# Kernel optimization log

Hardware: AMD Instinct MI355X
Metric: run time of the kernel (lower is better)

The kernel has to match this reference:

```python
import math
import jax, jax.numpy as jnp
import numpy as np
from jax import lax


def rotate_nearest(x, angle_deg):
    # x: (..., H, W); nearest-neighbor rotation about image center with expand=True
    H, W = x.shape[-2:]
    th = math.radians(angle_deg)
    c, s = math.cos(th), math.sin(th)
    nW = int(math.ceil(abs(W * c) + abs(H * s)))
    nH = int(math.ceil(abs(W * s) + abs(H * c)))
    cy, cx = (H - 1) * 0.5, (W - 1) * 0.5
    ncy, ncx = (nH - 1) * 0.5, (nW - 1) * 0.5
    yy, xx = jnp.meshgrid(jnp.arange(nH, dtype=jnp.float32), jnp.arange(nW, dtype=jnp.float32), indexing='ij')
    sx = c * (xx - ncx) - s * (yy - ncy) + cx
    sy = s * (xx - ncx) + c * (yy - ncy) + cy
    ix = jnp.clip(jnp.round(sx).astype(jnp.int32), 0, W - 1)
    iy = jnp.clip(jnp.round(sy).astype(jnp.int32), 0, H - 1)
    valid = (sx >= -0.5) & (sx <= W - 0.5) & (sy >= -0.5) & (sy <= H - 0.5)
    out = x[..., iy, ix]
    return jnp.where(valid, out, jnp.zeros((), dtype=x.dtype))


def scharr_gradients(img):
    # img: (B, C, H, W) -> (B, C, 2, H, W); cross-correlation like F.conv2d
    B, C, H, W = img.shape
    kx = jnp.array([[-3., 0., 3.], [10., 0., 10.], [-3., 0., 3.]], dtype=img.dtype)
    k = jnp.stack([kx, kx.T])[:, None]  # (2,1,3,3)
    y = lax.conv_general_dilated(img.reshape(B * C, 1, H, W), k, (1, 1), [(1, 1), (1, 1)],
                                 dimension_numbers=('NCHW', 'OIHW', 'NCHW'))
    return y.reshape(B, C, 2, H, W)


def rotated_xywh(img_height, img_width, angle=45.0):
    th = math.radians(angle)
    a, b = math.cos(th), math.sin(th)
    cx, cy = img_width / 2.0, img_height / 2.0
    rot = np.array([[a, b, (1 - a) * cx - b * cy], [-b, a, b * cx + (1 - a) * cy]])
    pts = np.array([[0, 0, 1], [img_width - 1, 0, 1], [0, img_height - 1, 1],
                    [img_width - 1, img_height - 1, 1]], dtype=np.float64)
    p = pts @ rot.T
    return (p[:, 0].min(), p[:, 1].min(), p[:, 0].max() - p[:, 0].min(), p[:, 1].max() - p[:, 1].min())


def gaussian_derivatives(img):
    # img: (C, H, W) -> (C, 8, H, W) : [grad+, grad-, rot_grad+, rot_grad-]
    C, H, W = img.shape
    g = scharr_gradients(img[None])[0]  # (C,2,H,W)
    xywh = rotated_xywh(H, W, 45.0)
    startx = int(max(0, (xywh[2] - W) / 2))
    starty = int(max(0, (xywh[3] - H) / 2))
    img_rot = rotate_nearest(img, 45.0)
    g_rot = scharr_gradients(img_rot[None])[0]
    g_rot = rotate_nearest(g_rot, -45.0)
    g_rot = g_rot[..., starty:starty + H, startx:startx + W]
    return jnp.concatenate([jnp.maximum(g, 0.0), jnp.minimum(g, 0.0),
                            jnp.maximum(g_rot, 0.0), jnp.minimum(g_rot, 0.0)], axis=-3)


def normalize_min_max(x):
    hmin = x.min(axis=(-2, -1), keepdims=True)
    hmax = x.max(axis=(-2, -1), keepdims=True)
    return (x - hmin) / (hmax - hmin)


def setup_inputs() -> dict:
    key = jax.random.key(0)
    k1, k2 = jax.random.split(key)
    img = jax.random.uniform(k1, (3, 1024, 1024), dtype=jnp.float32)
    reg_lab = jax.random.randint(k2, (1024, 1024), 0, 5000, dtype=jnp.int64)
    return {"img": img, "reg_lab": reg_lab, "nb_segs": 5000,
            "color_histogram_bins": 25, "texture_histogram_bins": 10}


def reference(img, reg_lab, nb_segs, color_histogram_bins, texture_histogram_bins):
    C, H, W = img.shape
    reg = reg_lab.reshape(-1).astype(jnp.int32)

    # per-region bounding boxes (vectorized segment min/max of pixel coords)
    yy, xx = jnp.meshgrid(jnp.arange(H, dtype=jnp.int32), jnp.arange(W, dtype=jnp.int32), indexing='ij')
    x_min = jax.ops.segment_min(xx.reshape(-1), reg, num_segments=nb_segs)
    y_min = jax.ops.segment_min(yy.reshape(-1), reg, num_segments=nb_segs)
    x_max = jax.ops.segment_max(xx.reshape(-1), reg, num_segments=nb_segs)
    y_max = jax.ops.segment_max(yy.reshape(-1), reg, num_segments=nb_segs)
    xywh = jnp.stack([x_min, y_min, x_max - x_min, y_max - y_min], axis=-1)  # (nb_segs, 4)

    region_sizes = jax.ops.segment_sum(jnp.ones_like(reg, jnp.float32), reg, num_segments=nb_segs)

    # color histograms
    cb = color_histogram_bins
    qc = (img * (cb - 1)).astype(jnp.int32)  # trunc == floor for x >= 0
    Zc = (reg_lab[None].astype(jnp.int32) * cb + qc).reshape(C, -1)
    hist_c = jax.vmap(lambda z: jax.ops.segment_sum(jnp.ones_like(z, jnp.float32), z, num_segments=nb_segs * cb))(Zc)
    color_hist = hist_c.reshape(C, nb_segs, cb).transpose(1, 0, 2)  # (nb_segs, C, cb)
    color_hist = color_hist / color_hist.sum(axis=(-2, -1), keepdims=True)

    # texture histograms over 8 gaussian-derivative channels
    tb = texture_histogram_bins
    deriv = normalize_min_max(gaussian_derivatives(img))  # (C, 8, H, W) in [0, 1]
    qt = (deriv * (tb - 1)).astype(jnp.int32)
    Zt = (reg_lab[None, None].astype(jnp.int32) * tb + qt).reshape(C * 8, -1)
    hist_t = jax.vmap(lambda z: jax.ops.segment_sum(jnp.ones_like(z, jnp.float32), z, num_segments=nb_segs * tb))(Zt)
    tex_hist = hist_t.reshape(C, 8, nb_segs, tb).transpose(2, 0, 1, 3)  # (nb_segs, C, 8, tb)
    tex_hist = tex_hist / tex_hist.sum(axis=(-3, -2, -1), keepdims=True)

    return xywh, region_sizes, color_hist, tex_hist
```

## Files before the change

### kernel.cpp

```cpp
#include <hip/hip_runtime.h>
#include <math.h>
#include <float.h>
#include <limits.h>

#define HH 1024
#define WW 1024
#define NPIX (HH*WW)
#define RH 1449
#define RW 1449
#define NBSEG 5000
#define START 211
#define NBLK_MM 2048

#define OUT_XYWH_OFF  0
#define OUT_SIZE_OFF  20000
#define OUT_COLOR_OFF 25000
#define OUT_TEX_OFF   400000
#define OUT_TOTAL     1600000


__global__ __launch_bounds__(256) void k_zero(int* __restrict__ cnt) {
  int i = blockIdx.x * 256 + threadIdx.x;
  if (i < 5120) cnt[i] = 0;
}

__global__ __launch_bounds__(256, 8) void k_mm(const float* __restrict__ img,
                                               const int* __restrict__ reg,
                                               int* __restrict__ cnt,
                                               int* __restrict__ rank,
                                               float4* __restrict__ grad4,
                                               float* __restrict__ pmin,
                                               float* __restrict__ pmax,
                                               float cb, float sb, float cf, float sf) {
  int tbase = blockIdx.x * 256 + threadIdx.x;
  float vmn[12], vmx[12];
  #pragma unroll
  for (int m = 0; m < 12; ++m) { vmn[m] = FLT_MAX; vmx[m] = -FLT_MAX; }

  #pragma unroll
  for (int k = 0; k < 2; ++k) {
    int p = tbase + k * (NPIX / 2);
    int y = p >> 10, x = p & (WW - 1);
    int s = reg[p];
    if ((unsigned)s < (unsigned)NBSEG) rank[p] = atomicAdd(&cnt[s], 1);

    float sx, sy;
    {
      #pragma clang fp contract(off)
      float dx = (float)(x + START) - 1024.5f;
      float dy = (float)(y + START) - 1024.5f;
      sx = cb*dx - sb*dy + 724.0f;
      sy = sb*dx + cb*dy + 724.0f;
    }
    bool valid2 = (sx >= -0.5f) && (sx <= (float)RW - 0.5f) &&
                  (sy >= -0.5f) && (sy <= (float)RH - 0.5f);
    int ix = min(max((int)rintf(sx), 0), RW - 1);
    int iy = min(max((int)rintf(sy), 0), RH - 1);

    float fxc, fyc;
    {
      #pragma clang fp contract(off)
      float ddx = (float)ix - 724.0f;
      float ddy = (float)iy - 724.0f;
      fxc = cf*ddx - sf*ddy + 511.5f;
      fyc = sf*ddx + cf*ddy + 511.5f;
    }

    int idxs[9];
    unsigned okm = 0;
    #pragma unroll
    for (int t = 0; t < 9; ++t) {
      const int dxi = (t % 3) - 1, dyi = (t / 3) - 1;
      int rx = ix + dxi, ry = iy + dyi;
      bool inside = ((unsigned)rx < (unsigned)RW) && ((unsigned)ry < (unsigned)RH);
      float fx = fxc + (cf*(float)dxi - sf*(float)dyi);
      float fy = fyc + (sf*(float)dxi + cf*(float)dyi);
      bool v1 = (fx >= -0.5f) && (fx <= 1023.5f) && (fy >= -0.5f) && (fy <= 1023.5f);
      int jx = min(max((int)rintf(fx), 0), WW - 1);
      int jy = min(max((int)rintf(fy), 0), HH - 1);
      idxs[t] = jy * WW + jx;
      okm |= ((unsigned)(inside && v1)) << t;
    }

    bool interior = (x >= 1) && (x <= WW - 2) && (y >= 1) && (y <= HH - 2);

    #pragma unroll
    for (int c = 0; c < 3; ++c) {
      const float* pp = img + (long)c * NPIX;
      float n00, n01, n02, n10, n12, n20, n21, n22;
      if (interior) {
        const float* q = pp + p;
        n00 = q[-WW - 1]; n01 = q[-WW]; n02 = q[-WW + 1];
        n10 = q[-1];                    n12 = q[1];
        n20 = q[WW - 1];  n21 = q[WW];  n22 = q[WW + 1];
      } else {
        bool yu = y > 0, yd = y < HH - 1, xl = x > 0, xr = x < WW - 1;
        n00 = (yu && xl) ? pp[p - WW - 1] : 0.0f;
        n01 = (yu)       ? pp[p - WW]     : 0.0f;
        n02 = (yu && xr) ? pp[p - WW + 1] : 0.0f;
        n10 = (xl)       ? pp[p - 1]      : 0.0f;
        n12 = (xr)       ? pp[p + 1]      : 0.0f;
        n20 = (yd && xl) ? pp[p + WW - 1] : 0.0f;
        n21 = (yd)       ? pp[p + WW]     : 0.0f;
        n22 = (yd && xr) ? pp[p + WW + 1] : 0.0f;
      }
      float a0 = -3.0f*n00 + 3.0f*n02 + 10.0f*n10 + 10.0f*n12 - 3.0f*n20 + 3.0f*n22;
      float a1 = -3.0f*n00 + 10.0f*n01 - 3.0f*n02 + 3.0f*n20 + 10.0f*n21 + 3.0f*n22;

      float m0, m1, m2, m3, m5, m6, m7, m8;
      m0 = (okm & 1u)   ? pp[idxs[0]] : 0.0f;
      m1 = (okm & 2u)   ? pp[idxs[1]] : 0.0f;
      m2 = (okm & 4u)   ? pp[idxs[2]] : 0.0f;
      m3 = (okm & 8u)   ? pp[idxs[3]] : 0.0f;
      m5 = (okm & 32u)  ? pp[idxs[5]] : 0.0f;
      m6 = (okm & 64u)  ? pp[idxs[6]] : 0.0f;
      m7 = (okm & 128u) ? pp[idxs[7]] : 0.0f;
      m8 = (okm & 256u) ? pp[idxs[8]] : 0.0f;
      float r0 = -3.0f*m0 + 3.0f*m2 + 10.0f*m3 + 10.0f*m5 - 3.0f*m6 + 3.0f*m8;
      float r1 = -3.0f*m0 + 10.0f*m1 - 3.0f*m2 + 3.0f*m6 + 10.0f*m7 + 3.0f*m8;
      float b0 = valid2 ? r0 : 0.0f;
      float b1 = valid2 ? r1 : 0.0f;

      grad4[(long)c * NPIX + p] = make_float4(a0, a1, b0, b1);

      vmn[2*c]     = fminf(vmn[2*c],     a0); vmx[2*c]     = fmaxf(vmx[2*c],     a0);
      vmn[2*c + 1] = fminf(vmn[2*c + 1], a1); vmx[2*c + 1] = fmaxf(vmx[2*c + 1], a1);
      vmn[6 + 2*c]     = fminf(vmn[6 + 2*c],     b0); vmx[6 + 2*c]     = fmaxf(vmx[6 + 2*c],     b0);
      vmn[6 + 2*c + 1] = fminf(vmn[6 + 2*c + 1], b1); vmx[6 + 2*c + 1] = fmaxf(vmx[6 + 2*c + 1], b1);
    }
  }

  #pragma unroll
  for (int off = 32; off >= 1; off >>= 1) {
    #pragma unroll
    for (int m = 0; m < 12; ++m) {
      vmn[m] = fminf(vmn[m], __shfl_xor(vmn[m], off));
      vmx[m] = fmaxf(vmx[m], __shfl_xor(vmx[m], off));
    }
  }
  __shared__ float smn[12][4], smx[12][4];
  int wv = threadIdx.x >> 6;
  if ((threadIdx.x & 63) == 0) {
    #pragma unroll
    for (int m = 0; m < 12; ++m) { smn[m][wv] = vmn[m]; smx[m][wv] = vmx[m]; }
  }
  __syncthreads();
  if (threadIdx.x < 12) {
    int m = threadIdx.x;
    float mn = fminf(fminf(smn[m][0], smn[m][1]), fminf(smn[m][2], smn[m][3]));
    float mx = fmaxf(fmaxf(smx[m][0], smx[m][1]), fmaxf(smx[m][2], smx[m][3]));
    pmin[m * NBLK_MM + blockIdx.x] = mn;
    pmax[m * NBLK_MM + blockIdx.x] = mx;
  }
}

__global__ __launch_bounds__(1024) void k_redscan(const float* __restrict__ pmin,
                                                  const float* __restrict__ pmax,
                                                  const int* __restrict__ cnt,
                                                  float* __restrict__ gmm,
                                                  int* __restrict__ start) {
  int t = threadIdx.x;
  if (blockIdx.x < 12) {
    int m = blockIdx.x;
    float mn = fminf(pmin[m * NBLK_MM + t], pmin[m * NBLK_MM + 1024 + t]);
    float mx = fmaxf(pmax[m * NBLK_MM + t], pmax[m * NBLK_MM + 1024 + t]);
    #pragma unroll
    for (int off = 32; off >= 1; off >>= 1) {
      mn = fminf(mn, __shfl_xor(mn, off));
      mx = fmaxf(mx, __shfl_xor(mx, off));
    }
    __shared__ float smn[16], smx[16];
    int wv = t >> 6;
    if ((t & 63) == 0) { smn[wv] = mn; smx[wv] = mx; }
    __syncthreads();
    if (t == 0) {
      #pragma unroll
      for (int i = 1; i < 16; ++i) { mn = fminf(mn, smn[i]); mx = fmaxf(mx, smx[i]); }
      gmm[2*m] = mn; gmm[2*m + 1] = mx;
    }
    return;
  }
  __shared__ int part[1024];
  int base = t * 5;
  int v[5]; int sum = 0;
  #pragma unroll
  for (int j = 0; j < 5; ++j) {
    v[j] = (base + j < NBSEG) ? cnt[base + j] : 0;
    sum += v[j];
  }
  part[t] = sum;
  __syncthreads();
  #pragma unroll
  for (int d = 1; d < 1024; d <<= 1) {
    int xv = (t >= d) ? part[t - d] : 0;
    __syncthreads();
    part[t] += xv;
    __syncthreads();
  }
  int run = (t > 0) ? part[t - 1] : 0;
  #pragma unroll
  for (int j = 0; j < 5; ++j) {
    int i = base + j;
    if (i <= NBSEG) start[i] = run;
    run += v[j];
  }
}

__global__ __launch_bounds__(256) void k_bin(const float* __restrict__ img,
                                             const int* __restrict__ reg,
                                             const int* __restrict__ rank,
                                             const int* __restrict__ start,
                                             const float* __restrict__ gmm,
                                             const float4* __restrict__ grad4,
                                             uint4* __restrict__ rec) {
  __shared__ float params[48];
  if (threadIdx.x < 24) {
    int t = threadIdx.x;
    int c = t / 8, k = t % 8;
    int b = (k < 4) ? (2*c + (k & 1)) : (6 + 2*c + (k & 1));
    bool pos = ((k >> 1) & 1) == 0;
    float mn = gmm[2*b], mx = gmm[2*b + 1];
    float hmin, hmax;
    if (pos) { hmin = fmaxf(mn, 0.0f); hmax = fmaxf(mx, 0.0f); }
    else     { hmin = fminf(mn, 0.0f); hmax = fminf(mx, 0.0f); }
    params[2*t]     = hmin;
    params[2*t + 1] = 9.0f / (hmax - hmin);
  }
  __syncthreads();

  int p = blockIdx.x * 256 + threadIdx.x;
  int s = reg[p];
  if ((unsigned)s >= (unsigned)NBSEG) return;

  unsigned q[24];
  #pragma unroll
  for (int c = 0; c < 3; ++c) {
    float4 g = grad4[(long)c * NPIX + p];
    float gv[2] = { g.x, g.y };
    float rv[2] = { g.z, g.w };
    #pragma unroll
    for (int d = 0; d < 2; ++d) {
      {
        int m = c*8 + d;
        float v = fmaxf(gv[d], 0.0f);
        int qq = (int)((v - params[2*m]) * params[2*m + 1]);
        q[m] = (unsigned)min(max(qq, 0), 9);
      }
      {
        int m = c*8 + 2 + d;
        float v = fminf(gv[d], 0.0f);
        int qq = (int)((v - params[2*m]) * params[2*m + 1]);
        q[m] = (unsigned)min(max(qq, 0), 9);
      }
      {
        int m = c*8 + 4 + d;
        float v = fmaxf(rv[d], 0.0f);
        int qq = (int)((v - params[2*m]) * params[2*m + 1]);
        q[m] = (unsigned)min(max(qq, 0), 9);
      }
      {
        int m = c*8 + 6 + d;
        float v = fminf(rv[d], 0.0f);
        int qq = (int)((v - params[2*m]) * params[2*m + 1]);
        q[m] = (unsigned)min(max(qq, 0), 9);
      }
    }
  }
  unsigned qc[3];
  #pragma unroll
  for (int c = 0; c < 3; ++c) {
    int cc = (int)(img[(long)c * NPIX + p] * 24.0f);
    qc[c] = (unsigned)min(max(cc, 0), 24);
  }

  unsigned trip[8];
  #pragma unroll
  for (int j = 0; j < 8; ++j)
    trip[j] = q[3*j] + 10u*q[3*j + 1] + 100u*q[3*j + 2];
  unsigned cp = qc[0] + 25u*qc[1] + 625u*qc[2];

  uint4 r;
  r.x = (unsigned)p | (trip[0] << 20);
  r.y = trip[1] | (trip[2] << 10) | (trip[3] << 20);
  r.z = trip[4] | (trip[5] << 10) | (trip[6] << 20);
  r.w = trip[7] | (cp << 10);

  rec[start[s] + rank[p]] = r;
}

__global__ __launch_bounds__(256) void k_accum(const uint4* __restrict__ rec,
                                               const int* __restrict__ start,
                                               float* __restrict__ out) {
  __shared__ unsigned hist[316];
  __shared__ int bb[4];
  int tid = threadIdx.x;
  int lane = tid & 63;

  for (int i = tid; i < 316; i += 256) hist[i] = 0;
  if (tid == 0) { bb[0] = INT_MAX; bb[1] = INT_MAX; bb[2] = INT_MIN; bb[3] = INT_MIN; }
  __syncthreads();

  int s = blockIdx.x;
  int beg = start[s], end = start[s + 1];
  int n = end - beg;

  unsigned acc[5] = {0, 0, 0, 0, 0};
  int xmn = INT_MAX, ymn = INT_MAX, xmx = INT_MIN, ymx = INT_MIN;

  for (int base2 = beg; base2 < end; base2 += 256) {
    int i = base2 + tid;
    bool act = i < end;
    uint4 r = rec[act ? i : beg];
    unsigned inv = act ? 0u : 0xFFu;

    unsigned tr[8];
    tr[0] = r.x >> 20;
    tr[1] = r.y & 0x3FFu; tr[2] = (r.y >> 10) & 0x3FFu; tr[3] = r.y >> 20;
    tr[4] = r.z & 0x3FFu; tr[5] = (r.z >> 10) & 0x3FFu; tr[6] = r.z >> 20;
    tr[7] = r.w & 0x3FFu;
    unsigned cp = r.w >> 10;

    unsigned qv[24];
    #pragma unroll
    for (int j = 0; j < 8; ++j) {
      unsigned t = tr[j];
      unsigned q2 = t / 100u; unsigned rr = t - 100u*q2;
      unsigned q1 = rr / 10u; unsigned q0 = rr - 10u*q1;
      qv[3*j]     = q0 | inv;
      qv[3*j + 1] = q1 | inv;
      qv[3*j + 2] = q2 | inv;
    }
    unsigned c0 = (cp % 25u) | inv;
    unsigned rem = cp / 25u;
    unsigned c1 = (rem % 25u) | inv;
    unsigned c2 = (rem / 25u) | inv;

    if (act) {
      unsigned p = r.x & 0xFFFFFu;
      int x = (int)(p & 1023u), y = (int)(p >> 10);
      xmn = min(xmn, x); ymn = min(ymn, y);
      xmx = max(xmx, x); ymx = max(ymx, y);
    }

    #pragma unroll
    for (int m = 0; m < 24; ++m) {
      #pragma unroll
      for (int b = 0; b < 10; ++b) {
        unsigned cntb = (unsigned)__popcll(__ballot(qv[m] == (unsigned)b));
        int idx = m * 10 + b;
        acc[idx >> 6] += (lane == (idx & 63)) ? cntb : 0u;
      }
    }
    unsigned qcs[3] = { c0, c1, c2 };
    #pragma unroll
    for (int cm = 0; cm < 3; ++cm) {
      #pragma unroll
      for (int b = 0; b < 25; ++b) {
        unsigned cntb = (unsigned)__popcll(__ballot(qcs[cm] == (unsigned)b));
        int idx = 240 + cm * 25 + b;
        acc[idx >> 6] += (lane == (idx & 63)) ? cntb : 0u;
      }
    }
  }

  #pragma unroll
  for (int j = 0; j < 5; ++j) {
    int idx = j * 64 + lane;
    if (idx < 315 && acc[j]) atomicAdd(&hist[idx], acc[j]);
  }

  #pragma unroll
  for (int off = 32; off >= 1; off >>= 1) {
    xmn = min(xmn, __shfl_xor(xmn, off));
    ymn = min(ymn, __shfl_xor(ymn, off));
    xmx = max(xmx, __shfl_xor(xmx, off));
    ymx = max(ymx, __shfl_xor(ymx, off));
  }
  if (lane == 0) {
    atomicMin(&bb[0], xmn); atomicMin(&bb[1], ymn);
    atomicMax(&bb[2], xmx); atomicMax(&bb[3], ymx);
  }
  __syncthreads();

  if (tid == 0) {
    out[4*s + 0] = (float)bb[0];
    out[4*s + 1] = (float)bb[1];
    out[4*s + 2] = (float)(bb[2] - bb[0]);
    out[4*s + 3] = (float)(bb[3] - bb[1]);
    out[OUT_SIZE_OFF + s] = (float)n;
  }
  bool ok = n > 0;
  float cden = 3.0f * (float)n, tden = 24.0f * (float)n;
  for (int i = tid; i < 240; i += 256)
    out[OUT_TEX_OFF + s*240 + i] = ok ? (float)hist[i] / tden : 0.0f;
  for (int i = tid; i < 75; i += 256)
    out[OUT_COLOR_OFF + s*75 + i] = ok ? (float)hist[240 + i] / cden : 0.0f;
}


extern "C" void kernel_launch(void* const* d_in, const int* in_sizes, int n_in,
                              void* d_out, int out_size, void* d_ws, size_t ws_size,
                              hipStream_t stream) {
  const float* img = (const float*)d_in[0];
  const int*   reg = (const int*)d_in[1];
  float* out = (float*)d_out;

  char* ws = (char*)d_ws;
  size_t off = 0;
  float4* grad4 = (float4*)(ws + off); off += (size_t)3 * NPIX * 16;  off = (off + 255) & ~(size_t)255;
  uint4*  rec   = (uint4*)(ws + off);  off += (size_t)(NPIX + 256) * 16; off = (off + 255) & ~(size_t)255;
  int*    rank  = (int*)(ws + off);    off += (size_t)NPIX * 4;       off = (off + 255) & ~(size_t)255;
  int*    cnt   = (int*)(ws + off);    off += 5120 * 4;
  int*    start = (int*)(ws + off);    off += 5008 * 4;
  float*  gmm   = (float*)(ws + off);  off += 32 * 4;                 off = (off + 255) & ~(size_t)255;
  float*  pmin  = (float*)(ws + off);  off += (size_t)12 * NBLK_MM * 4;
  float*  pmax  = (float*)(ws + off);  off += (size_t)12 * NBLK_MM * 4;
  (void)ws_size; (void)in_sizes; (void)n_in; (void)out_size;

  double th  = 45.0 * (M_PI / 180.0);
  float cf = (float)cos(th),  sf = (float)sin(th);
  double thb = -45.0 * (M_PI / 180.0);
  float cbk = (float)cos(thb), sbk = (float)sin(thb);

  k_zero   <<<20,        256,  0, stream>>>(cnt);
  k_mm     <<<NBLK_MM,   256,  0, stream>>>(img, reg, cnt, rank, grad4, pmin, pmax, cbk, sbk, cf, sf);
  k_redscan<<<13,        1024, 0, stream>>>(pmin, pmax, cnt, gmm, start);
  k_bin    <<<NPIX/256,  256,  0, stream>>>(img, reg, rank, start, gmm, grad4, rec);
  k_accum  <<<NBSEG,     256,  0, stream>>>(rec, start, out);
}
```

Before: 224.7 us.

## Store gradients as truncated bf16 and precompute color bin codes in gradient kernel

The gradient intermediate buffer is stored as bf16 by truncation (8 bytes per pixel-channel instead of 16), and min/max are computed on the rounded values so bin ranges stay consistent. The color quantization code is computed in k_mm from the already loaded center pixel and written as a 16-bit array, so k_bin no longer rereads the image. Interior stencil loads are vectorized. This cuts intermediate memory traffic, but the reduced gradient precision can move values across histogram bin edges relative to the fp32 reference.

```diff
diff --git a/kernel.cpp b/kernel.cpp
--- a/kernel.cpp
+++ b/kernel.cpp
@@ -18,6 +18,16 @@
 #define OUT_TEX_OFF   400000
 #define OUT_TOTAL     1600000
 
+typedef float f32x4 __attribute__((ext_vector_type(4), aligned(4)));
+typedef float f32x2 __attribute__((ext_vector_type(2), aligned(4)));
+
+__device__ __forceinline__ unsigned bf16t(float v) {
+  return __float_as_uint(v) >> 16;
+}
+__device__ __forceinline__ float bf16f(unsigned h) {
+  return __uint_as_float(h << 16);
+}
+
 
 __global__ __launch_bounds__(256) void k_zero(int* __restrict__ cnt) {
   int i = blockIdx.x * 256 + threadIdx.x;
@@ -28,7 +38,8 @@
                                                const int* __restrict__ reg,
                                                int* __restrict__ cnt,
                                                int* __restrict__ rank,
-                                               float4* __restrict__ grad4,
+                                               uint2* __restrict__ grad2,
+                                               unsigned short* __restrict__ cpq,
                                                float* __restrict__ pmin,
                                                float* __restrict__ pmax,
                                                float cb, float sb, float cf, float sf) {
@@ -84,15 +95,20 @@
 
     bool interior = (x >= 1) && (x <= WW - 2) && (y >= 1) && (y <= HH - 2);
 
+    unsigned qc[3];
     #pragma unroll
     for (int c = 0; c < 3; ++c) {
       const float* pp = img + (long)c * NPIX;
-      float n00, n01, n02, n10, n12, n20, n21, n22;
+      float n00, n01, n02, n10, n12, n20, n21, n22, ctr;
       if (interior) {
         const float* q = pp + p;
-        n00 = q[-WW - 1]; n01 = q[-WW]; n02 = q[-WW + 1];
-        n10 = q[-1];                    n12 = q[1];
-        n20 = q[WW - 1];  n21 = q[WW];  n22 = q[WW + 1];
+        f32x4 ru = *(const f32x4*)(q - WW - 1);
+        f32x4 rm = *(const f32x4*)(q - 1);
+        f32x2 rd = *(const f32x2*)(q + WW - 1);
+        n00 = ru.x; n01 = ru.y; n02 = ru.z;
+        n10 = rm.x; ctr = rm.y; n12 = rm.z;
+        n20 = rd.x; n21 = rd.y;
+        n22 = q[WW + 1];
       } else {
         bool yu = y > 0, yd = y < HH - 1, xl = x > 0, xr = x < WW - 1;
         n00 = (yu && xl) ? pp[p - WW - 1] : 0.0f;
@@ -103,6 +119,7 @@
         n20 = (yd && xl) ? pp[p + WW - 1] : 0.0f;
         n21 = (yd)       ? pp[p + WW]     : 0.0f;
         n22 = (yd && xr) ? pp[p + WW + 1] : 0.0f;
+        ctr = pp[p];
       }
       float a0 = -3.0f*n00 + 3.0f*n02 + 10.0f*n10 + 10.0f*n12 - 3.0f*n20 + 3.0f*n22;
       float a1 = -3.0f*n00 + 10.0f*n01 - 3.0f*n02 + 3.0f*n20 + 10.0f*n21 + 3.0f*n22;
@@ -121,13 +138,20 @@
       float b0 = valid2 ? r0 : 0.0f;
       float b1 = valid2 ? r1 : 0.0f;
 
-      grad4[(long)c * NPIX + p] = make_float4(a0, a1, b0, b1);
-
-      vmn[2*c]     = fminf(vmn[2*c],     a0); vmx[2*c]     = fmaxf(vmx[2*c],     a0);
-      vmn[2*c + 1] = fminf(vmn[2*c + 1], a1); vmx[2*c + 1] = fmaxf(vmx[2*c + 1], a1);
-      vmn[6 + 2*c]     = fminf(vmn[6 + 2*c],     b0); vmx[6 + 2*c]     = fmaxf(vmx[6 + 2*c],     b0);
-      vmn[6 + 2*c + 1] = fminf(vmn[6 + 2*c + 1], b1); vmx[6 + 2*c + 1] = fmaxf(vmx[6 + 2*c + 1], b1);
-    }
+      unsigned ua0 = bf16t(a0), ua1 = bf16t(a1), ub0 = bf16t(b0), ub1 = bf16t(b1);
+      float a0r = bf16f(ua0), a1r = bf16f(ua1), b0r = bf16f(ub0), b1r = bf16f(ub1);
+
+      grad2[(long)c * NPIX + p] = make_uint2(ua0 | (ua1 << 16), ub0 | (ub1 << 16));
+
+      int cc = (int)(ctr * 24.0f);
+      qc[c] = (unsigned)min(max(cc, 0), 24);
+
+      vmn[2*c]     = fminf(vmn[2*c],     a0r); vmx[2*c]     = fmaxf(vmx[2*c],     a0r);
+      vmn[2*c + 1] = fminf(vmn[2*c + 1], a1r); vmx[2*c + 1] = fmaxf(vmx[2*c + 1], a1r);
+      vmn[6 + 2*c]     = fminf(vmn[6 + 2*c],     b0r); vmx[6 + 2*c]     = fmaxf(vmx[6 + 2*c],     b0r);
+      vmn[6 + 2*c + 1] = fminf(vmn[6 + 2*c + 1], b1r); vmx[6 + 2*c + 1] = fmaxf(vmx[6 + 2*c + 1], b1r);
+    }
+    cpq[p] = (unsigned short)(qc[0] + 25u*qc[1] + 625u*qc[2]);
   }
 
   #pragma unroll
@@ -206,12 +230,12 @@
   }
 }
 
-__global__ __launch_bounds__(256) void k_bin(const float* __restrict__ img,
-                                             const int* __restrict__ reg,
+__global__ __launch_bounds__(256) void k_bin(const int* __restrict__ reg,
                                              const int* __restrict__ rank,
                                              const int* __restrict__ start,
                                              const float* __restrict__ gmm,
-                                             const float4* __restrict__ grad4,
+                                             const uint2* __restrict__ grad2,
+                                             const unsigned short* __restrict__ cpq,
                                              uint4* __restrict__ rec) {
   __shared__ float params[48];
   if (threadIdx.x < 24) {
@@ -235,9 +259,9 @@
   unsigned q[24];
   #pragma unroll
   for (int c = 0; c < 3; ++c) {
-    float4 g = grad4[(long)c * NPIX + p];
-    float gv[2] = { g.x, g.y };
-    float rv[2] = { g.z, g.w };
+    uint2 g = grad2[(long)c * NPIX + p];
+    float gv[2] = { bf16f(g.x & 0xFFFFu), __uint_as_float(g.x & 0xFFFF0000u) };
+    float rv[2] = { bf16f(g.y & 0xFFFFu), __uint_as_float(g.y & 0xFFFF0000u) };
     #pragma unroll
     for (int d = 0; d < 2; ++d) {
       {
@@ -266,18 +290,12 @@
       }
     }
   }
-  unsigned qc[3];
-  #pragma unroll
-  for (int c = 0; c < 3; ++c) {
-    int cc = (int)(img[(long)c * NPIX + p] * 24.0f);
-    qc[c] = (unsigned)min(max(cc, 0), 24);
-  }
 
   unsigned trip[8];
   #pragma unroll
   for (int j = 0; j < 8; ++j)
     trip[j] = q[3*j] + 10u*q[3*j + 1] + 100u*q[3*j + 2];
-  unsigned cp = qc[0] + 25u*qc[1] + 625u*qc[2];
+  unsigned cp = (unsigned)cpq[p];
 
   uint4 r;
   r.x = (unsigned)p | (trip[0] << 20);
@@ -407,9 +425,10 @@
 
   char* ws = (char*)d_ws;
   size_t off = 0;
-  float4* grad4 = (float4*)(ws + off); off += (size_t)3 * NPIX * 16;  off = (off + 255) & ~(size_t)255;
+  uint2*  grad2 = (uint2*)(ws + off);  off += (size_t)3 * NPIX * 8;   off = (off + 255) & ~(size_t)255;
   uint4*  rec   = (uint4*)(ws + off);  off += (size_t)(NPIX + 256) * 16; off = (off + 255) & ~(size_t)255;
   int*    rank  = (int*)(ws + off);    off += (size_t)NPIX * 4;       off = (off + 255) & ~(size_t)255;
+  unsigned short* cpq = (unsigned short*)(ws + off); off += (size_t)NPIX * 2; off = (off + 255) & ~(size_t)255;
   int*    cnt   = (int*)(ws + off);    off += 5120 * 4;
   int*    start = (int*)(ws + off);    off += 5008 * 4;
   float*  gmm   = (float*)(ws + off);  off += 32 * 4;                 off = (off + 255) & ~(size_t)255;
@@ -423,8 +442,8 @@
   float cbk = (float)cos(thb), sbk = (float)sin(thb);
 
   k_zero   <<<20,        256,  0, stream>>>(cnt);
-  k_mm     <<<NBLK_MM,   256,  0, stream>>>(img, reg, cnt, rank, grad4, pmin, pmax, cbk, sbk, cf, sf);
+  k_mm     <<<NBLK_MM,   256,  0, stream>>>(img, reg, cnt, rank, grad2, cpq, pmin, pmax, cbk, sbk, cf, sf);
   k_redscan<<<13,        1024, 0, stream>>>(pmin, pmax, cnt, gmm, start);
-  k_bin    <<<NPIX/256,  256,  0, stream>>>(img, reg, rank, start, gmm, grad4, rec);
+  k_bin    <<<NPIX/256,  256,  0, stream>>>(reg, rank, start, gmm, grad2, cpq, rec);
   k_accum  <<<NBSEG,     256,  0, stream>>>(rec, start, out);
 }
```

After: 221.9 us. About the same (-1.2%).
